# Optimization experiments

Hardware: AMD Instinct MI355X
Metric: run time of the kernel (lower is better)

The kernel has to match this reference:

```python
import jax, jax.numpy as jnp
import numpy as np

D_MODEL = 1024
NUM_HEADS = 16
HEAD_DIM = D_MODEL // NUM_HEADS
NEG_INF = -1e9


def setup_inputs() -> dict:
    key = jax.random.key(0)
    ks = jax.random.split(key, 9)
    B, S, SI = 4, 1024, 512
    scale = 1.0 / np.sqrt(D_MODEL)
    return {
        "hidden_states": jax.random.normal(ks[0], (B, S, D_MODEL), jnp.float32),
        "image_hidden_states": jax.random.normal(ks[1], (B, SI, D_MODEL), jnp.float32),
        "attention_mask": jax.random.randint(ks[2], (B, 1, S, S + SI), 0, 2, jnp.int32),
        "w_q": jax.random.normal(ks[3], (D_MODEL, D_MODEL), jnp.float32) * scale,
        "w_k": jax.random.normal(ks[4], (D_MODEL, D_MODEL), jnp.float32) * scale,
        "w_v": jax.random.normal(ks[5], (D_MODEL, D_MODEL), jnp.float32) * scale,
        "u_k": jax.random.normal(ks[6], (D_MODEL, D_MODEL), jnp.float32) * scale,
        "u_v": jax.random.normal(ks[7], (D_MODEL, D_MODEL), jnp.float32) * scale,
        "w_o": jax.random.normal(ks[8], (D_MODEL, D_MODEL), jnp.float32) * scale,
    }


def _split_heads(x):
    # [B, S, D] -> [B, H, S, Dh]
    B, S, _ = x.shape
    return x.reshape(B, S, NUM_HEADS, HEAD_DIM).transpose(0, 2, 1, 3)


def reference(hidden_states, image_hidden_states, attention_mask,
              w_q, w_k, w_v, u_k, u_v, w_o):
    # nn.Linear(bias=False): y = x @ W.T
    q = _split_heads(hidden_states @ w_q.T)          # [B,H,S,Dh]
    k = _split_heads(hidden_states @ w_k.T)          # [B,H,S,Dh]
    v = _split_heads(hidden_states @ w_v.T)
    k_img = _split_heads(image_hidden_states @ u_k.T)  # [B,H,SI,Dh]
    v_img = _split_heads(image_hidden_states @ u_v.T)
    k = jnp.concatenate([k, k_img], axis=2)          # [B,H,S+SI,Dh]
    v = jnp.concatenate([v, v_img], axis=2)

    scores = jnp.einsum('bhqd,bhkd->bhqk', q, k) / np.sqrt(HEAD_DIM)
    scores = jnp.where(attention_mask == 0, NEG_INF, scores)
    p_attn = jax.nn.softmax(scores, axis=-1)         # dropout p=0.0 (eval)
    x = jnp.einsum('bhqk,bhkd->bhqd', p_attn, v)     # [B,H,S,Dh]
    B, H, S, Dh = x.shape
    x = x.transpose(0, 2, 1, 3).reshape(B, S, D_MODEL)
    return x @ w_o.T
```

## Files before the change

### kernel.cpp

```cpp
#include <hip/hip_runtime.h>
#include <stdint.h>


typedef unsigned short u16;
typedef short bf16x8v __attribute__((ext_vector_type(8)));
typedef float f32x4 __attribute__((ext_vector_type(4)));

__device__ __forceinline__ u16 f2bf(float f) {
  union { float f; uint32_t u; } x; x.f = f;
  uint32_t r = x.u + 0x7FFFu + ((x.u >> 16) & 1u);
  return (u16)(r >> 16);
}

__device__ __forceinline__ uint32_t cvtpk(float a, float b) {
  uint32_t r;
  asm("v_cvt_pk_bf16_f32 %0, %1, %2" : "=v"(r) : "v"(a), "v"(b));
  return r;
}

__device__ __forceinline__ float maskand(float e, uint32_t msrc, int off) {
  uint32_t mm = (uint32_t)((int32_t)(msrc << (31 - off)) >> 31);
  union { float f; uint32_t u; } x; x.f = e; x.u &= mm; return x.f;
}

__device__ __forceinline__ void gl_lds16(const u16* g, u16* l) {
  __builtin_amdgcn_global_load_lds((const __attribute__((address_space(1))) unsigned int*)g,
                                   (__attribute__((address_space(3))) unsigned int*)l,
                                   16, 0, 0);
}

__global__ __launch_bounds__(256) void prep(const int* __restrict__ mk,
                                            const float4* __restrict__ hs,
                                            const float4* __restrict__ im,
                                            const float4* __restrict__ w0, const float4* __restrict__ w1,
                                            const float4* __restrict__ w2, const float4* __restrict__ w3,
                                            const float4* __restrict__ w4, const float4* __restrict__ w5,
                                            uint32_t* __restrict__ Mw,
                                            u16* __restrict__ Hb, u16* __restrict__ Ib,
                                            u16* __restrict__ Wb) {
  const int nthr = gridDim.x * 256;
  const int gid = blockIdx.x * 256 + threadIdx.x;

  for (int w = gid; w < 196608; w += nthr) {
    const int4* p = (const int4*)(mk + (size_t)w * 32);
    uint32_t bits = 0;
    #pragma unroll
    for (int c = 0; c < 8; ++c) {
      int4 v = p[c];
      bits |= (uint32_t)(v.x != 0) << (4 * c);
      bits |= (uint32_t)(v.y != 0) << (4 * c + 1);
      bits |= (uint32_t)(v.z != 0) << (4 * c + 2);
      bits |= (uint32_t)(v.w != 0) << (4 * c + 3);
    }
    Mw[w] = bits;
  }
  for (int i = gid; i < 1572864; i += nthr) {
    float4 v; u16* d;
    if (i < 1048576) { v = hs[i];            d = Hb + (size_t)i * 4; }
    else             { v = im[i - 1048576];  d = Ib + (size_t)(i - 1048576) * 4; }
    ushort4 o; o.x = f2bf(v.x); o.y = f2bf(v.y); o.z = f2bf(v.z); o.w = f2bf(v.w);
    *(ushort4*)d = o;
  }
  for (int i = gid; i < 1572864; i += nthr) {
    int w = i >> 18, off = i & 262143;
    const float4* s;
    switch (w) {
      case 0: s = w0; break; case 1: s = w1; break; case 2: s = w2; break;
      case 3: s = w3; break; case 4: s = w4; break; default: s = w5; break;
    }
    float4 v = s[off];
    ushort4 o; o.x = f2bf(v.x); o.y = f2bf(v.y); o.z = f2bf(v.z); o.w = f2bf(v.w);
    *(ushort4*)(Wb + ((size_t)w << 20) + (size_t)off * 4) = o;
  }
}

__global__ __launch_bounds__(512, 2) void gemm_qkv(const u16* __restrict__ Hb, const u16* __restrict__ Ib,
                                                   const u16* __restrict__ Wb,
                                                   u16* __restrict__ Qd, u16* __restrict__ Kd,
                                                   u16* __restrict__ Vd)
{
  __shared__ __align__(16) u16 As[2 * 16384];
  __shared__ __align__(16) u16 Bs[2 * 16384];
  const int hb = blockIdx.x;
  const int xcd = hb & 7, slot = hb >> 3;
  int bid;
  if (slot < 24) bid = xcd * 24 + slot;
  else           bid = 192 + xcd * 8 + (slot - 24);
  const u16 *A, *Bm;
  int bm, bn, mode;
  if (bid < 192) { mode = 4; A = Hb; Bm = Wb;
                   bm = (bid / 12) * 256; bn = (bid % 12) * 256; }
  else           { mode = 5; A = Ib; Bm = Wb + 3 * 1048576;
                   int r = bid - 192; bm = (r >> 3) * 256; bn = (r & 7) * 256; }
  const int tid = threadIdx.x, lane = tid & 63, wave = tid >> 6;
  const int wr = wave >> 2, wc = wave & 3;
  const int g = lane >> 4, c = lane & 15, cs = c & 7;
  const int srow = tid >> 3;
  const int pch  = tid & 7;
  const int swz  = (pch ^ (srow & 7)) * 8;

  f32x4 zf = {0.f, 0.f, 0.f, 0.f};
  f32x4 acc[8][4];
  #pragma unroll
  for (int f = 0; f < 8; ++f)
    #pragma unroll
    for (int nf = 0; nf < 4; ++nf) acc[f][nf] = zf;

  #define STG_ALL(buf, kt)                                                          \
    do {                                                                            \
      _Pragma("unroll")                                                             \
      for (int j_ = 0; j_ < 4; ++j_) {                                              \
        int row_ = j_ * 64 + srow;                                                  \
        gl_lds16(A + (size_t)(bm + row_) * 1024 + (kt) * 64 + swz,                  \
                 &As[(buf) + row_ * 64 + pch * 8]);                                 \
      }                                                                             \
      _Pragma("unroll")                                                             \
      for (int j_ = 0; j_ < 4; ++j_) {                                              \
        int row_ = j_ * 64 + srow;                                                  \
        gl_lds16(Bm + (size_t)(bn + row_) * 1024 + (kt) * 64 + swz,                 \
                 &Bs[(buf) + row_ * 64 + pch * 8]);                                 \
      }                                                                             \
    } while (0)

  STG_ALL(0, 0);
  asm volatile("s_waitcnt vmcnt(0)" ::: "memory");
  asm volatile("s_barrier" ::: "memory");

  for (int kt = 0; kt < 16; ++kt) {
    const int bc = (kt & 1) * 16384;
    const int bx = bc ^ 16384;
    if (kt < 15) STG_ALL(bx, kt + 1);

    bf16x8v Bf[4][2];
    #pragma unroll
    for (int nf = 0; nf < 4; ++nf)
      #pragma unroll
      for (int ks = 0; ks < 2; ++ks)
        Bf[nf][ks] = *(const bf16x8v*)&Bs[bc + (wc * 64 + nf * 16 + c) * 64 + ((ks * 4 + g) ^ cs) * 8];

    #pragma unroll
    for (int p = 0; p < 4; ++p) {
      bf16x8v Af[2][2];
      #pragma unroll
      for (int i = 0; i < 2; ++i)
        #pragma unroll
        for (int ks = 0; ks < 2; ++ks)
          Af[i][ks] = *(const bf16x8v*)&As[bc + (wr * 128 + (p * 2 + i) * 16 + c) * 64 + ((ks * 4 + g) ^ cs) * 8];
      __builtin_amdgcn_s_setprio(1);
      #pragma unroll
      for (int i = 0; i < 2; ++i)
        #pragma unroll
        for (int nf = 0; nf < 4; ++nf)
          #pragma unroll
          for (int ks = 0; ks < 2; ++ks)
            acc[p * 2 + i][nf] =
              __builtin_amdgcn_mfma_f32_16x16x32_bf16(Af[i][ks], Bf[nf][ks], acc[p * 2 + i][nf], 0, 0, 0);
      __builtin_amdgcn_s_setprio(0);
    }

    if (kt < 15) {
      asm volatile("s_waitcnt vmcnt(0)" ::: "memory");
      asm volatile("s_barrier" ::: "memory");
    }
  }
  #undef STG_ALL

  #pragma unroll
  for (int f = 0; f < 8; ++f) {
    #pragma unroll
    for (int nf = 0; nf < 4; ++nf) {
      #pragma unroll
      for (int j = 0; j < 4; ++j) {
        int gm = bm + wr * 128 + f * 16 + 4 * g + j;
        int gn = bn + wc * 64 + nf * 16 + c;
        float v = acc[f][nf][j];
        if (mode == 4) {
          int b_ = gm >> 10, s_ = gm & 1023;
          if (gn < 1024)      Qd[(size_t)gm * 1024 + gn] = f2bf(v * 0.18033688011112042f);
          else if (gn < 2048) Kd[(size_t)(b_ * 1536 + s_) * 1024 + (gn - 1024)] = f2bf(v);
          else                Vd[(size_t)(b_ * 1024 + (gn - 2048)) * 1536 + s_] = f2bf(v);
        } else {
          int b_ = gm >> 9, s_ = gm & 511;
          if (gn < 1024) Kd[(size_t)(b_ * 1536 + 1024 + s_) * 1024 + gn] = f2bf(v);
          else           Vd[(size_t)(b_ * 1024 + (gn - 1024)) * 1536 + 1024 + s_] = f2bf(v);
        }
      }
    }
  }
}

__global__ __launch_bounds__(256) void gemm_out(const u16* __restrict__ A, const u16* __restrict__ Bm,
                                                float* __restrict__ Cout)
{
  __shared__ __align__(16) u16 As[2 * 8192];
  __shared__ __align__(16) u16 Bs[2 * 8192];
  const int hb = blockIdx.x;
  const int xcd = hb & 7, slot = hb >> 3;
  const int rg = xcd * 4 + (slot >> 3);
  const int cg = slot & 7;
  const int bm = rg * 128, bn = cg * 128;
  const int tid  = threadIdx.x;
  const int lane = tid & 63, wave = tid >> 6;
  const int wr = wave >> 1, wc = wave & 1;
  const int g = lane >> 4, c = lane & 15, cs = c & 7;
  const int sr  = tid >> 3;
  const int pch = tid & 7;
  const int swz = (pch ^ (sr & 7)) * 8;

  f32x4 zf = {0.f, 0.f, 0.f, 0.f};
  f32x4 acc[4][4];
  #pragma unroll
  for (int mi = 0; mi < 4; ++mi)
    #pragma unroll
    for (int ni = 0; ni < 4; ++ni) acc[mi][ni] = zf;

  #define STGO(buf, kt)                                                             \
    do {                                                                            \
      _Pragma("unroll")                                                             \
      for (int q_ = 0; q_ < 4; ++q_) {                                              \
        int row_ = q_ * 32 + sr;                                                    \
        gl_lds16(A + (size_t)(bm + row_) * 1024 + (kt) * 64 + swz,                  \
                 &As[(buf) + row_ * 64 + pch * 8]);                                 \
      }                                                                             \
      _Pragma("unroll")                                                             \
      for (int q_ = 0; q_ < 4; ++q_) {                                              \
        int row_ = q_ * 32 + sr;                                                    \
        gl_lds16(Bm + (size_t)(bn + row_) * 1024 + (kt) * 64 + swz,                 \
                 &Bs[(buf) + row_ * 64 + pch * 8]);                                 \
      }                                                                             \
    } while (0)

  STGO(0, 0);
  asm volatile("s_waitcnt vmcnt(0)" ::: "memory");
  asm volatile("s_barrier" ::: "memory");

  for (int kt = 0; kt < 16; ++kt) {
    const int bc = (kt & 1) * 8192;
    const int bx = bc ^ 8192;
    if (kt < 15) STGO(bx, kt + 1);

    #pragma unroll
    for (int ks = 0; ks < 2; ++ks) {
      bf16x8v af[4], bfr[4];
      #pragma unroll
      for (int mi = 0; mi < 4; ++mi)
        af[mi] = *(const bf16x8v*)&As[bc + (wr * 64 + mi * 16 + c) * 64 + ((ks * 4 + g) ^ cs) * 8];
      #pragma unroll
      for (int ni = 0; ni < 4; ++ni)
        bfr[ni] = *(const bf16x8v*)&Bs[bc + (wc * 64 + ni * 16 + c) * 64 + ((ks * 4 + g) ^ cs) * 8];
      __builtin_amdgcn_s_setprio(1);
      #pragma unroll
      for (int mi = 0; mi < 4; ++mi)
        #pragma unroll
        for (int ni = 0; ni < 4; ++ni)
          acc[mi][ni] = __builtin_amdgcn_mfma_f32_16x16x32_bf16(af[mi], bfr[ni], acc[mi][ni], 0, 0, 0);
      __builtin_amdgcn_s_setprio(0);
    }

    if (kt < 15) {
      asm volatile("s_waitcnt vmcnt(0)" ::: "memory");
      asm volatile("s_barrier" ::: "memory");
    }
  }
  #undef STGO

  #pragma unroll
  for (int mi = 0; mi < 4; ++mi)
    #pragma unroll
    for (int ni = 0; ni < 4; ++ni)
      #pragma unroll
      for (int j = 0; j < 4; ++j) {
        int gm = bm + wr * 64 + mi * 16 + 4 * g + j;
        int gn = bn + wc * 64 + ni * 16 + c;
        Cout[(size_t)gm * 1024 + gn] = acc[mi][ni][j];
      }
}

__global__ __launch_bounds__(256) void attn_kernel(const u16* __restrict__ Q, const u16* __restrict__ Kc,
                                                   const u16* __restrict__ Vt,
                                                   const uint32_t* __restrict__ Mw,
                                                   u16* __restrict__ AO)
{
  const int bid = blockIdx.x;
  const int grp = bid & 63;
  const int qt  = bid >> 6;
  const int h = grp & 15, b = grp >> 4;
  const int q0 = qt * 64;
  const int tid = threadIdx.x, lane = tid & 63, wave = tid >> 6;
  const int g = lane >> 4, c = lane & 15;
  const int qw = q0 + wave * 16;

  __shared__ __align__(16) u16 Ks[64 * 64];
  __shared__ __align__(16) u16 Vs[64 * 64];
  __shared__ __align__(16) u16 Ps[4][16 * 72];

  bf16x8v qf0, qf1;
  {
    const u16* qp = Q + (size_t)(b * 1024 + qw + c) * 1024 + h * 64 + g * 8;
    qf0 = *(const bf16x8v*)qp;
    qf1 = *(const bf16x8v*)(qp + 32);
  }
  f32x4 zf = {0.f, 0.f, 0.f, 0.f};
  f32x4 O[4];
  float l = 0.f;
  #pragma unroll
  for (int dt = 0; dt < 4; ++dt) O[dt] = zf;

  const int sr  = tid >> 3;
  const int pch = tid & 7;
  const int swz = (pch ^ (sr & 7)) * 8;
  const int cs  = c & 7;
  const u16* Kbase = Kc + (size_t)(b * 1536) * 1024 + h * 64;
  const u16* Vbase = Vt + (size_t)(b * 1024 + h * 64) * 1536;
  const uint32_t* mrow = Mw + (size_t)(b * 1024 + qw + c) * 48;

  bf16x8v kr0, kr1, vr0, vr1;
  kr0 = *(const bf16x8v*)(Kbase + (size_t)sr * 1024 + pch * 8);
  kr1 = *(const bf16x8v*)(Kbase + (size_t)(32 + sr) * 1024 + pch * 8);
  vr0 = *(const bf16x8v*)(Vbase + (size_t)sr * 1536 + pch * 8);
  vr1 = *(const bf16x8v*)(Vbase + (size_t)(32 + sr) * 1536 + pch * 8);
  *(bf16x8v*)&Ks[sr * 64 + swz]        = kr0;
  *(bf16x8v*)&Ks[(32 + sr) * 64 + swz] = kr1;
  *(bf16x8v*)&Vs[sr * 64 + swz]        = vr0;
  *(bf16x8v*)&Vs[(32 + sr) * 64 + swz] = vr1;
  __syncthreads();

  for (int kt = 0; kt < 24; ++kt) {
    if (kt < 23) {
      const int ln = (kt + 1) * 64;
      kr0 = *(const bf16x8v*)(Kbase + (size_t)(ln + sr) * 1024 + pch * 8);
      kr1 = *(const bf16x8v*)(Kbase + (size_t)(ln + 32 + sr) * 1024 + pch * 8);
      vr0 = *(const bf16x8v*)(Vbase + (size_t)sr * 1536 + ln + pch * 8);
      vr1 = *(const bf16x8v*)(Vbase + (size_t)(32 + sr) * 1536 + ln + pch * 8);
    }
    uint2 mwv = *(const uint2*)(mrow + kt * 2);

    f32x4 s[4];
    __builtin_amdgcn_s_setprio(1);
    #pragma unroll
    for (int nt = 0; nt < 4; ++nt) {
      const u16* kr = &Ks[(nt * 16 + c) * 64];
      bf16x8v k0 = *(const bf16x8v*)&kr[(g ^ cs) * 8];
      bf16x8v k1 = *(const bf16x8v*)&kr[((4 + g) ^ cs) * 8];
      f32x4 z = zf;
      z = __builtin_amdgcn_mfma_f32_16x16x32_bf16(k0, qf0, z, 0, 0, 0);
      z = __builtin_amdgcn_mfma_f32_16x16x32_bf16(k1, qf1, z, 0, 0, 0);
      s[nt] = z;
    }
    __builtin_amdgcn_s_setprio(0);

    uint64_t mq = (((uint64_t)mwv.y << 32) | (uint64_t)mwv.x) >> (4 * g);
    uint32_t mlo = (uint32_t)mq, mhi = (uint32_t)(mq >> 32);
    #pragma unroll
    for (int nt = 0; nt < 4; ++nt) {
      uint32_t msrc = (nt < 2) ? mlo : mhi;
      #pragma unroll
      for (int j = 0; j < 4; ++j) {
        float e = exp2f(s[nt][j]);
        float p = maskand(e, msrc, 16 * (nt & 1) + j);
        s[nt][j] = p;
        l += p;
      }
    }

    u16* pw = &Ps[wave][0];
    #pragma unroll
    for (int nt = 0; nt < 4; ++nt) {
      uint2 pk2;
      pk2.x = cvtpk(s[nt][0], s[nt][1]);
      pk2.y = cvtpk(s[nt][2], s[nt][3]);
      *(uint2*)&pw[c * 72 + nt * 16 + g * 4] = pk2;
    }
    bf16x8v pb0 = *(const bf16x8v*)&pw[c * 72 + g * 8];
    bf16x8v pb1 = *(const bf16x8v*)&pw[c * 72 + 32 + g * 8];
    __builtin_amdgcn_s_setprio(1);
    #pragma unroll
    for (int dt = 0; dt < 4; ++dt) {
      const u16* vr = &Vs[(dt * 16 + c) * 64];
      bf16x8v v0 = *(const bf16x8v*)&vr[(g ^ cs) * 8];
      bf16x8v v1 = *(const bf16x8v*)&vr[((4 + g) ^ cs) * 8];
      O[dt] = __builtin_amdgcn_mfma_f32_16x16x32_bf16(v0, pb0, O[dt], 0, 0, 0);
      O[dt] = __builtin_amdgcn_mfma_f32_16x16x32_bf16(v1, pb1, O[dt], 0, 0, 0);
    }
    __builtin_amdgcn_s_setprio(0);

    __syncthreads();
    if (kt < 23) {
      *(bf16x8v*)&Ks[sr * 64 + swz]        = kr0;
      *(bf16x8v*)&Ks[(32 + sr) * 64 + swz] = kr1;
      *(bf16x8v*)&Vs[sr * 64 + swz]        = vr0;
      *(bf16x8v*)&Vs[(32 + sr) * 64 + swz] = vr1;
      __syncthreads();
    }
  }

  float r = l;
  r += __shfl_xor(r, 16);
  r += __shfl_xor(r, 32);
  float inv = 1.f / r;
  size_t ro = (size_t)(b * 1024 + qw + c) * 1024 + h * 64;
  #pragma unroll
  for (int dt = 0; dt < 4; ++dt) {
    uint2 st;
    st.x = cvtpk(O[dt][0] * inv, O[dt][1] * inv);
    st.y = cvtpk(O[dt][2] * inv, O[dt][3] * inv);
    *(uint2*)&AO[ro + dt * 16 + 4 * g] = st;
  }
}

extern "C" void kernel_launch(void* const* d_in, const int* in_sizes, int n_in,
                              void* d_out, int out_size, void* d_ws, size_t ws_size,
                              hipStream_t stream) {
  (void)in_sizes; (void)n_in; (void)out_size; (void)ws_size;
  const float* hs = (const float*)d_in[0];
  const float* im = (const float*)d_in[1];
  const int*   mk = (const int*)d_in[2];
  const float* wq = (const float*)d_in[3];
  const float* wk = (const float*)d_in[4];
  const float* wv = (const float*)d_in[5];
  const float* uk = (const float*)d_in[6];
  const float* uv = (const float*)d_in[7];
  const float* wo = (const float*)d_in[8];

  char* ws = (char*)d_ws;
  u16* Hb  = (u16*)(ws + 0);
  u16* Ib  = (u16*)(ws + 8388608);
  u16* Wb  = (u16*)(ws + 12582912);
  u16* Qb  = (u16*)(ws + 25165824);
  u16* Kb  = (u16*)(ws + 33554432);
  u16* Vtb = (u16*)(ws + 46137344);
  uint32_t* Mw = (uint32_t*)(ws + 58720256);

  prep<<<2048, 256, 0, stream>>>(mk, (const float4*)hs, (const float4*)im,
                                 (const float4*)wq, (const float4*)wk, (const float4*)wv,
                                 (const float4*)uk, (const float4*)uv, (const float4*)wo,
                                 Mw, Hb, Ib, Wb);
  gemm_qkv<<<256, 512, 0, stream>>>(Hb, Ib, Wb, Qb, Kb, Vtb);
  attn_kernel<<<1024, 256, 0, stream>>>(Qb, Kb, Vtb, Mw, Hb);
  gemm_out<<<256, 256, 0, stream>>>(Hb, Wb + 5 * 1048576, (float*)d_out);
}
```

Measured before the change: 160.0 us.

## Fuse fp32-to-bf16 conversion into GEMM tile loads, drop separate prep pass

```diff
diff --git a/kernel.cpp b/kernel.cpp
--- a/kernel.cpp
+++ b/kernel.cpp
@@ -29,75 +29,47 @@
                                    16, 0, 0);
 }
 
-__global__ __launch_bounds__(256) void prep(const int* __restrict__ mk,
-                                            const float4* __restrict__ hs,
-                                            const float4* __restrict__ im,
-                                            const float4* __restrict__ w0, const float4* __restrict__ w1,
-                                            const float4* __restrict__ w2, const float4* __restrict__ w3,
-                                            const float4* __restrict__ w4, const float4* __restrict__ w5,
-                                            uint32_t* __restrict__ Mw,
-                                            u16* __restrict__ Hb, u16* __restrict__ Ib,
-                                            u16* __restrict__ Wb) {
-  const int nthr = gridDim.x * 256;
-  const int gid = blockIdx.x * 256 + threadIdx.x;
-
-  for (int w = gid; w < 196608; w += nthr) {
-    const int4* p = (const int4*)(mk + (size_t)w * 32);
-    uint32_t bits = 0;
-    #pragma unroll
-    for (int c = 0; c < 8; ++c) {
-      int4 v = p[c];
-      bits |= (uint32_t)(v.x != 0) << (4 * c);
-      bits |= (uint32_t)(v.y != 0) << (4 * c + 1);
-      bits |= (uint32_t)(v.z != 0) << (4 * c + 2);
-      bits |= (uint32_t)(v.w != 0) << (4 * c + 3);
-    }
-    Mw[w] = bits;
-  }
-  for (int i = gid; i < 1572864; i += nthr) {
-    float4 v; u16* d;
-    if (i < 1048576) { v = hs[i];            d = Hb + (size_t)i * 4; }
-    else             { v = im[i - 1048576];  d = Ib + (size_t)(i - 1048576) * 4; }
-    ushort4 o; o.x = f2bf(v.x); o.y = f2bf(v.y); o.z = f2bf(v.z); o.w = f2bf(v.w);
-    *(ushort4*)d = o;
-  }
-  for (int i = gid; i < 1572864; i += nthr) {
-    int w = i >> 18, off = i & 262143;
-    const float4* s;
-    switch (w) {
-      case 0: s = w0; break; case 1: s = w1; break; case 2: s = w2; break;
-      case 3: s = w3; break; case 4: s = w4; break; default: s = w5; break;
-    }
-    float4 v = s[off];
-    ushort4 o; o.x = f2bf(v.x); o.y = f2bf(v.y); o.z = f2bf(v.z); o.w = f2bf(v.w);
-    *(ushort4*)(Wb + ((size_t)w << 20) + (size_t)off * 4) = o;
-  }
-}
-
-__global__ __launch_bounds__(512, 2) void gemm_qkv(const u16* __restrict__ Hb, const u16* __restrict__ Ib,
-                                                   const u16* __restrict__ Wb,
-                                                   u16* __restrict__ Qd, u16* __restrict__ Kd,
-                                                   u16* __restrict__ Vd)
+__global__ __launch_bounds__(256) void mask_pack(const int* __restrict__ mk,
+                                                 uint32_t* __restrict__ Mw) {
+  int w = blockIdx.x * 256 + threadIdx.x;
+  const int4* p = (const int4*)(mk + (size_t)w * 32);
+  uint32_t bits = 0;
+  #pragma unroll
+  for (int c = 0; c < 8; ++c) {
+    int4 v = p[c];
+    bits |= (uint32_t)(v.x != 0) << (4 * c);
+    bits |= (uint32_t)(v.y != 0) << (4 * c + 1);
+    bits |= (uint32_t)(v.z != 0) << (4 * c + 2);
+    bits |= (uint32_t)(v.w != 0) << (4 * c + 3);
+  }
+  Mw[w] = bits;
+}
+
+__global__ __launch_bounds__(512, 2) void gemm_qkv(
+    const float* __restrict__ Hs, const float* __restrict__ Im,
+    const float* __restrict__ Wq, const float* __restrict__ Wk, const float* __restrict__ Wv,
+    const float* __restrict__ Uk, const float* __restrict__ Uv,
+    u16* __restrict__ Qd, u16* __restrict__ Kd, u16* __restrict__ Vd)
 {
   __shared__ __align__(16) u16 As[2 * 16384];
   __shared__ __align__(16) u16 Bs[2 * 16384];
   const int hb = blockIdx.x;
   const int xcd = hb & 7, slot = hb >> 3;
-  int bid;
-  if (slot < 24) bid = xcd * 24 + slot;
-  else           bid = 192 + xcd * 8 + (slot - 24);
-  const u16 *A, *Bm;
+  int bid = (slot < 24) ? xcd * 24 + slot : 192 + xcd * 8 + (slot - 24);
+  const float *Ap, *Bp;
   int bm, bn, mode;
-  if (bid < 192) { mode = 4; A = Hb; Bm = Wb;
-                   bm = (bid / 12) * 256; bn = (bid % 12) * 256; }
-  else           { mode = 5; A = Ib; Bm = Wb + 3 * 1048576;
-                   int r = bid - 192; bm = (r >> 3) * 256; bn = (r & 7) * 256; }
+  if (bid < 192) { mode = 4; bm = (bid / 12) * 256; bn = (bid % 12) * 256;
+                   Ap = Hs + (size_t)bm * 1024;
+                   Bp = ((bn < 1024) ? Wq : (bn < 2048) ? Wk : Wv) + (size_t)(bn & 1023) * 1024; }
+  else           { mode = 5; int r = bid - 192; bm = (r >> 3) * 256; bn = (r & 7) * 256;
+                   Ap = Im + (size_t)bm * 1024;
+                   Bp = ((bn < 1024) ? Uk : Uv) + (size_t)(bn & 1023) * 1024; }
   const int tid = threadIdx.x, lane = tid & 63, wave = tid >> 6;
   const int wr = wave >> 2, wc = wave & 3;
   const int g = lane >> 4, c = lane & 15, cs = c & 7;
   const int srow = tid >> 3;
   const int pch  = tid & 7;
-  const int swz  = (pch ^ (srow & 7)) * 8;
+  const int gsw  = (pch ^ (srow & 7)) * 8;
 
   f32x4 zf = {0.f, 0.f, 0.f, 0.f};
   f32x4 acc[8][4];
@@ -106,30 +78,51 @@
     #pragma unroll
     for (int nf = 0; nf < 4; ++nf) acc[f][nf] = zf;
 
-  #define STG_ALL(buf, kt)                                                          \
-    do {                                                                            \
-      _Pragma("unroll")                                                             \
-      for (int j_ = 0; j_ < 4; ++j_) {                                              \
-        int row_ = j_ * 64 + srow;                                                  \
-        gl_lds16(A + (size_t)(bm + row_) * 1024 + (kt) * 64 + swz,                  \
-                 &As[(buf) + row_ * 64 + pch * 8]);                                 \
-      }                                                                             \
-      _Pragma("unroll")                                                             \
-      for (int j_ = 0; j_ < 4; ++j_) {                                              \
-        int row_ = j_ * 64 + srow;                                                  \
-        gl_lds16(Bm + (size_t)(bn + row_) * 1024 + (kt) * 64 + swz,                 \
-                 &Bs[(buf) + row_ * 64 + pch * 8]);                                 \
-      }                                                                             \
-    } while (0)
-
-  STG_ALL(0, 0);
-  asm volatile("s_waitcnt vmcnt(0)" ::: "memory");
-  asm volatile("s_barrier" ::: "memory");
+  float4 sa[4][2], sb[4][2];
+
+  #define LOAD_A(kt)                                                               \
+    _Pragma("unroll")                                                              \
+    for (int j_ = 0; j_ < 4; ++j_) {                                               \
+      const float* p_ = Ap + (size_t)(j_ * 64 + srow) * 1024 + (kt) * 64 + gsw;    \
+      sa[j_][0] = *(const float4*)p_;                                              \
+      sa[j_][1] = *(const float4*)(p_ + 4);                                        \
+    }
+  #define LOAD_B(kt)                                                               \
+    _Pragma("unroll")                                                              \
+    for (int j_ = 0; j_ < 4; ++j_) {                                               \
+      const float* p_ = Bp + (size_t)(j_ * 64 + srow) * 1024 + (kt) * 64 + gsw;    \
+      sb[j_][0] = *(const float4*)p_;                                              \
+      sb[j_][1] = *(const float4*)(p_ + 4);                                        \
+    }
+  #define CVT_A(buf)                                                               \
+    _Pragma("unroll")                                                              \
+    for (int j_ = 0; j_ < 4; ++j_) {                                               \
+      uint4 w_;                                                                    \
+      w_.x = cvtpk(sa[j_][0].x, sa[j_][0].y);                                      \
+      w_.y = cvtpk(sa[j_][0].z, sa[j_][0].w);                                      \
+      w_.z = cvtpk(sa[j_][1].x, sa[j_][1].y);                                      \
+      w_.w = cvtpk(sa[j_][1].z, sa[j_][1].w);                                      \
+      *(uint4*)&As[(buf) + (j_ * 64 + srow) * 64 + pch * 8] = w_;                  \
+    }
+  #define CVT_B(buf)                                                               \
+    _Pragma("unroll")                                                              \
+    for (int j_ = 0; j_ < 4; ++j_) {                                               \
+      uint4 w_;                                                                    \
+      w_.x = cvtpk(sb[j_][0].x, sb[j_][0].y);                                      \
+      w_.y = cvtpk(sb[j_][0].z, sb[j_][0].w);                                      \
+      w_.z = cvtpk(sb[j_][1].x, sb[j_][1].y);                                      \
+      w_.w = cvtpk(sb[j_][1].z, sb[j_][1].w);                                      \
+      *(uint4*)&Bs[(buf) + (j_ * 64 + srow) * 64 + pch * 8] = w_;                  \
+    }
+
+  LOAD_A(0); LOAD_B(0);
+  CVT_A(0);  CVT_B(0);
+  __syncthreads();
 
   for (int kt = 0; kt < 16; ++kt) {
     const int bc = (kt & 1) * 16384;
     const int bx = bc ^ 16384;
-    if (kt < 15) STG_ALL(bx, kt + 1);
+    if (kt < 15) LOAD_A(kt + 1);
 
     bf16x8v Bf[4][2];
     #pragma unroll
@@ -156,14 +149,23 @@
             acc[p * 2 + i][nf] =
               __builtin_amdgcn_mfma_f32_16x16x32_bf16(Af[i][ks], Bf[nf][ks], acc[p * 2 + i][nf], 0, 0, 0);
       __builtin_amdgcn_s_setprio(0);
-    }
-
+      if (p == 1 && kt < 15) {
+        __builtin_amdgcn_sched_barrier(0);
+        CVT_A(bx);
+        LOAD_B(kt + 1);
+        __builtin_amdgcn_sched_barrier(0);
+      }
+    }
     if (kt < 15) {
-      asm volatile("s_waitcnt vmcnt(0)" ::: "memory");
-      asm volatile("s_barrier" ::: "memory");
-    }
-  }
-  #undef STG_ALL
+      __builtin_amdgcn_sched_barrier(0);
+      CVT_B(bx);
+    }
+    __syncthreads();
+  }
+  #undef LOAD_A
+  #undef LOAD_B
+  #undef CVT_A
+  #undef CVT_B
 
   #pragma unroll
   for (int f = 0; f < 8; ++f) {
@@ -189,11 +191,11 @@
   }
 }
 
-__global__ __launch_bounds__(256) void gemm_out(const u16* __restrict__ A, const u16* __restrict__ Bm,
+__global__ __launch_bounds__(256) void gemm_out(const u16* __restrict__ A, const float* __restrict__ Bw,
                                                 float* __restrict__ Cout)
 {
-  __shared__ __align__(16) u16 As[2 * 8192];
-  __shared__ __align__(16) u16 Bs[2 * 8192];
+  __shared__ __align__(16) u16 As2[2 * 8192];
+  __shared__ __align__(16) u16 Bs2[2 * 8192];
   const int hb = blockIdx.x;
   const int xcd = hb & 7, slot = hb >> 3;
   const int rg = xcd * 4 + (slot >> 3);
@@ -205,7 +207,7 @@
   const int g = lane >> 4, c = lane & 15, cs = c & 7;
   const int sr  = tid >> 3;
   const int pch = tid & 7;
-  const int swz = (pch ^ (sr & 7)) * 8;
+  const int gsw = (pch ^ (sr & 7)) * 8;
 
   f32x4 zf = {0.f, 0.f, 0.f, 0.f};
   f32x4 acc[4][4];
@@ -214,40 +216,52 @@
     #pragma unroll
     for (int ni = 0; ni < 4; ++ni) acc[mi][ni] = zf;
 
-  #define STGO(buf, kt)                                                             \
-    do {                                                                            \
-      _Pragma("unroll")                                                             \
-      for (int q_ = 0; q_ < 4; ++q_) {                                              \
-        int row_ = q_ * 32 + sr;                                                    \
-        gl_lds16(A + (size_t)(bm + row_) * 1024 + (kt) * 64 + swz,                  \
-                 &As[(buf) + row_ * 64 + pch * 8]);                                 \
-      }                                                                             \
-      _Pragma("unroll")                                                             \
-      for (int q_ = 0; q_ < 4; ++q_) {                                              \
-        int row_ = q_ * 32 + sr;                                                    \
-        gl_lds16(Bm + (size_t)(bn + row_) * 1024 + (kt) * 64 + swz,                 \
-                 &Bs[(buf) + row_ * 64 + pch * 8]);                                 \
-      }                                                                             \
-    } while (0)
-
-  STGO(0, 0);
-  asm volatile("s_waitcnt vmcnt(0)" ::: "memory");
-  asm volatile("s_barrier" ::: "memory");
+  float4 sb[4][2];
+
+  #define STG_A(buf, kt)                                                           \
+    _Pragma("unroll")                                                              \
+    for (int q_ = 0; q_ < 4; ++q_) {                                               \
+      int row_ = q_ * 32 + sr;                                                     \
+      gl_lds16(A + (size_t)(bm + row_) * 1024 + (kt) * 64 + gsw,                   \
+               &As2[(buf) + row_ * 64 + pch * 8]);                                 \
+    }
+  #define LOAD_B(kt)                                                               \
+    _Pragma("unroll")                                                              \
+    for (int q_ = 0; q_ < 4; ++q_) {                                               \
+      const float* p_ = Bw + (size_t)(bn + q_ * 32 + sr) * 1024 + (kt) * 64 + gsw; \
+      sb[q_][0] = *(const float4*)p_;                                              \
+      sb[q_][1] = *(const float4*)(p_ + 4);                                        \
+    }
+  #define CVT_B(buf)                                                               \
+    _Pragma("unroll")                                                              \
+    for (int q_ = 0; q_ < 4; ++q_) {                                               \
+      uint4 w_;                                                                    \
+      w_.x = cvtpk(sb[q_][0].x, sb[q_][0].y);                                      \
+      w_.y = cvtpk(sb[q_][0].z, sb[q_][0].w);                                      \
+      w_.z = cvtpk(sb[q_][1].x, sb[q_][1].y);                                      \
+      w_.w = cvtpk(sb[q_][1].z, sb[q_][1].w);                                      \
+      *(uint4*)&Bs2[(buf) + (q_ * 32 + sr) * 64 + pch * 8] = w_;                   \
+    }
+
+  STG_A(0, 0);
+  LOAD_B(0);
+  CVT_B(0);
+  __syncthreads();
 
   for (int kt = 0; kt < 16; ++kt) {
     const int bc = (kt & 1) * 8192;
     const int bx = bc ^ 8192;
-    if (kt < 15) STGO(bx, kt + 1);
+    if (kt < 15) { STG_A(bx, kt + 1); LOAD_B(kt + 1); }
 
     #pragma unroll
     for (int ks = 0; ks < 2; ++ks) {
       bf16x8v af[4], bfr[4];
       #pragma unroll
       for (int mi = 0; mi < 4; ++mi)
-        af[mi] = *(const bf16x8v*)&As[bc + (wr * 64 + mi * 16 + c) * 64 + ((ks * 4 + g) ^ cs) * 8];
+        af[mi] = *(const bf16x8v*)&As2[bc + (wr * 64 + mi * 16 + c) * 64 + ((ks * 4 + g) ^ cs) * 8];
       #pragma unroll
       for (int ni = 0; ni < 4; ++ni)
-        bfr[ni] = *(const bf16x8v*)&Bs[bc + (wc * 64 + ni * 16 + c) * 64 + ((ks * 4 + g) ^ cs) * 8];
+        bfr[ni] = *(const bf16x8v*)&Bs2[bc + (wc * 64 + ni * 16 + c) * 64 + ((ks * 4 + g) ^ cs) * 8];
       __builtin_amdgcn_s_setprio(1);
       #pragma unroll
       for (int mi = 0; mi < 4; ++mi)
@@ -256,13 +270,15 @@
           acc[mi][ni] = __builtin_amdgcn_mfma_f32_16x16x32_bf16(af[mi], bfr[ni], acc[mi][ni], 0, 0, 0);
       __builtin_amdgcn_s_setprio(0);
     }
-
     if (kt < 15) {
-      asm volatile("s_waitcnt vmcnt(0)" ::: "memory");
-      asm volatile("s_barrier" ::: "memory");
-    }
-  }
-  #undef STGO
+      __builtin_amdgcn_sched_barrier(0);
+      CVT_B(bx);
+    }
+    __syncthreads();
+  }
+  #undef STG_A
+  #undef LOAD_B
+  #undef CVT_B
 
   #pragma unroll
   for (int mi = 0; mi < 4; ++mi)
@@ -423,19 +439,14 @@
   const float* wo = (const float*)d_in[8];
 
   char* ws = (char*)d_ws;
-  u16* Hb  = (u16*)(ws + 0);
-  u16* Ib  = (u16*)(ws + 8388608);
-  u16* Wb  = (u16*)(ws + 12582912);
-  u16* Qb  = (u16*)(ws + 25165824);
-  u16* Kb  = (u16*)(ws + 33554432);
-  u16* Vtb = (u16*)(ws + 46137344);
-  uint32_t* Mw = (uint32_t*)(ws + 58720256);
-
-  prep<<<2048, 256, 0, stream>>>(mk, (const float4*)hs, (const float4*)im,
-                                 (const float4*)wq, (const float4*)wk, (const float4*)wv,
-                                 (const float4*)uk, (const float4*)uv, (const float4*)wo,
-                                 Mw, Hb, Ib, Wb);
-  gemm_qkv<<<256, 512, 0, stream>>>(Hb, Ib, Wb, Qb, Kb, Vtb);
-  attn_kernel<<<1024, 256, 0, stream>>>(Qb, Kb, Vtb, Mw, Hb);
-  gemm_out<<<256, 256, 0, stream>>>(Hb, Wb + 5 * 1048576, (float*)d_out);
-}
+  u16* Qb  = (u16*)(ws + 0);
+  u16* Kb  = (u16*)(ws + 8388608);
+  u16* Vtb = (u16*)(ws + 20971520);
+  u16* AO  = (u16*)(ws + 33554432);
+  uint32_t* Mw = (uint32_t*)(ws + 41943040);
+
+  mask_pack<<<768, 256, 0, stream>>>(mk, Mw);
+  gemm_qkv<<<256, 512, 0, stream>>>(hs, im, wq, wk, wv, uk, uv, Qb, Kb, Vtb);
+  attn_kernel<<<1024, 256, 0, stream>>>(Qb, Kb, Vtb, Mw, AO);
+  gemm_out<<<256, 256, 0, stream>>>(AO, wo, (float*)d_out);
+}
```

Measured after the change: 158.9 us. Within noise of the previous version (-0.7%).
